# Performance work log

Measured on AMD Instinct MI355X. Metric: run time of the kernel, lower is better.

## Reference

```python
import jax, jax.numpy as jnp
import numpy as np

DIM = 768
N_HEADS = 12
HEAD_DIM = DIM // N_HEADS
B, S = 2, 4096


def setup_inputs() -> dict:
    key = jax.random.key(0)
    k_x, k_wqkv, k_bqkv, k_wout, k_bout = jax.random.split(key, 5)
    scale_in = 1.0 / np.sqrt(DIM)
    return {
        "x": jax.random.normal(k_x, (B, S, DIM), dtype=jnp.float32),
        "Wqkv": jax.random.normal(k_wqkv, (DIM, 3 * DIM), dtype=jnp.float32) * scale_in,
        "bqkv": jax.random.normal(k_bqkv, (3 * DIM,), dtype=jnp.float32) * 0.02,
        "Wout": jax.random.normal(k_wout, (DIM, DIM), dtype=jnp.float32) * scale_in,
        "bout": jax.random.normal(k_bout, (DIM,), dtype=jnp.float32) * 0.02,
    }


def reference(x, Wqkv, bqkv, Wout, bout):
    b, s, d = x.shape
    qkv = (x @ Wqkv + bqkv).reshape(b, s, 3, N_HEADS, HEAD_DIM)
    qkv = jnp.transpose(qkv, (2, 0, 3, 1, 4))  # [3, B, H, S, hd]
    q, k, v = qkv[0], qkv[1], qkv[2]
    scale = HEAD_DIM ** -0.5
    attn = jnp.einsum('bhqd,bhkd->bhqk', q, k) * scale  # [B, H, S, S]
    causal_mask = jnp.triu(jnp.ones((s, s), dtype=bool), k=1)
    attn = jnp.where(causal_mask[None, None], -jnp.inf, attn)
    attn = jax.nn.softmax(attn, axis=-1)
    out = jnp.einsum('bhqk,bhkd->bhqd', attn, v)  # [B, H, S, hd]
    out = jnp.transpose(out, (0, 2, 1, 3)).reshape(b, s, d)
    return out @ Wout + bout
```

## Files before the change

kernel.cpp:

```cpp
#include <hip/hip_runtime.h>
#include <hip/hip_bf16.h>
#include <math.h>

#define DIM 768
#define NH 12
#define HD 64
#define BATCH 2
#define SEQ 4096
#define MTOT (BATCH * SEQ)

#define QSCALE 0.1803368801111244f

typedef unsigned short u16;
typedef __bf16 bf16x8 __attribute__((ext_vector_type(8)));
typedef float  f32x4  __attribute__((ext_vector_type(4)));
typedef float  f32x16 __attribute__((ext_vector_type(16)));
typedef unsigned short u16x4 __attribute__((ext_vector_type(4)));
typedef unsigned short u16x8 __attribute__((ext_vector_type(8)));
typedef unsigned u32x4 __attribute__((ext_vector_type(4)));

__device__ inline u16 f2bf(float f) {
    unsigned u = __builtin_bit_cast(unsigned, f);
    u += 0x7fffu + ((u >> 16) & 1u);
    return (u16)(u >> 16);
}

#if defined(__has_builtin) && __has_builtin(__builtin_amdgcn_cvt_pk_bf16_f32)
#define HAVE_PK_BF16 1
__device__ inline unsigned pk2bf(float a, float b) {
    auto v = __builtin_amdgcn_cvt_pk_bf16_f32(a, b);
    return __builtin_bit_cast(unsigned, v);
}
#else
#define HAVE_PK_BF16 0
__device__ inline unsigned pk2bf(float a, float b) {
    return (unsigned)f2bf(a) | ((unsigned)f2bf(b) << 16);
}
#endif

__device__ inline f32x4 mfma16(bf16x8 a, bf16x8 b, f32x4 c) {
    return __builtin_amdgcn_mfma_f32_16x16x32_bf16(a, b, c, 0, 0, 0);
}
__device__ inline f32x16 mfma32(bf16x8 a, bf16x8 b, f32x16 c) {
    return __builtin_amdgcn_mfma_f32_32x32x16_bf16(a, b, c, 0, 0, 0);
}

__device__ inline void gl2lds16(const u16* g, u16* l) {
    __builtin_amdgcn_global_load_lds(
        (const __attribute__((address_space(1))) void*)g,
        (__attribute__((address_space(3))) void*)l,
        16, 0, 0);
}

__global__ __launch_bounds__(256)
void cvt_bf16(const float* __restrict__ src, u16* __restrict__ dst, int n8)
{
    int i = blockIdx.x * 256 + threadIdx.x;
    if (i >= n8) return;
    float4 a = ((const float4*)src)[i * 2];
    float4 b = ((const float4*)src)[i * 2 + 1];
    u16x8 o;
    o[0] = f2bf(a.x); o[1] = f2bf(a.y); o[2] = f2bf(a.z); o[3] = f2bf(a.w);
    o[4] = f2bf(b.x); o[5] = f2bf(b.y); o[6] = f2bf(b.z); o[7] = f2bf(b.w);
    ((u16x8*)dst)[i] = o;
}

__global__ __launch_bounds__(256)
void transpose_to_bf16(const float* __restrict__ src, u16* __restrict__ dst,
                       int R, int C)
{
    __shared__ float tile[32][33];
    const int c0 = blockIdx.x * 32, r0 = blockIdx.y * 32;
    const int tx = threadIdx.x & 31, ty = threadIdx.x >> 5;
#pragma unroll
    for (int i = 0; i < 4; ++i) {
        int row = ty * 4 + i;
        tile[row][tx] = src[(size_t)(r0 + row) * C + c0 + tx];
    }
    __syncthreads();
#pragma unroll
    for (int i = 0; i < 4; ++i) {
        int crow = ty * 4 + i;
        dst[(size_t)(c0 + crow) * R + r0 + tx] = f2bf(tile[tx][crow]);
    }
}

__device__ inline void gemm_lds_mainloop(const u16* __restrict__ Ag,
                                         const u16* __restrict__ Bg,
                                         int m0, int n0, int w, int lane,
                                         u16 (*As)[64 * 64], u16 (*Bs)[64 * 64],
                                         f32x4 acc[4][4])
{
    const int quad = lane >> 4, lc = lane & 15;
    const int wm = (w & 1) * 64, wn = (w >> 1) * 64;
    const int drow = lane >> 3;
    const int dp   = lane & 7;

#pragma unroll
    for (int mi = 0; mi < 4; ++mi)
#pragma unroll
        for (int nj = 0; nj < 4; ++nj)
            acc[mi][nj] = f32x4{0.f, 0.f, 0.f, 0.f};

#pragma unroll
    for (int i = 0; i < 2; ++i) {
        const int r  = w * 16 + i * 8 + drow;
        const int g  = dp ^ (r & 7);
        const int tr = 2 * r + (g >> 2);
        const int kc = g & 3;
        gl2lds16(Ag + (size_t)(m0 + tr) * 768 + kc * 8, &As[0][(w * 16 + i * 8) * 64]);
        gl2lds16(Bg + (size_t)(n0 + tr) * 768 + kc * 8, &Bs[0][(w * 16 + i * 8) * 64]);
    }
    __syncthreads();

    for (int ks = 0; ks < 24; ++ks) {
        const int cur = ks & 1;

        if (ks < 23) {
            const int k0n = (ks + 1) * 32;
#pragma unroll
            for (int i = 0; i < 2; ++i) {
                const int r  = w * 16 + i * 8 + drow;
                const int g  = dp ^ (r & 7);
                const int tr = 2 * r + (g >> 2);
                const int kc = g & 3;
                gl2lds16(Ag + (size_t)(m0 + tr) * 768 + k0n + kc * 8,
                         &As[1 - cur][(w * 16 + i * 8) * 64]);
                gl2lds16(Bg + (size_t)(n0 + tr) * 768 + k0n + kc * 8,
                         &Bs[1 - cur][(w * 16 + i * 8) * 64]);
            }
        }

        bf16x8 af[4], bfr[4];
#pragma unroll
        for (int mi = 0; mi < 4; ++mi) {
            const int m = wm + mi * 16 + lc;
            const int r = m >> 1;
            const int p = (((m & 1) * 4 + quad)) ^ (r & 7);
            af[mi] = *(const bf16x8*)&As[cur][r * 64 + p * 8];
        }
#pragma unroll
        for (int nj = 0; nj < 4; ++nj) {
            const int n = wn + nj * 16 + lc;
            const int r = n >> 1;
            const int p = (((n & 1) * 4 + quad)) ^ (r & 7);
            bfr[nj] = *(const bf16x8*)&Bs[cur][r * 64 + p * 8];
        }

#pragma unroll
        for (int mi = 0; mi < 4; ++mi)
#pragma unroll
            for (int nj = 0; nj < 4; ++nj)
                acc[mi][nj] = mfma16(af[mi], bfr[nj], acc[mi][nj]);

        __syncthreads();
    }
}

__global__ __launch_bounds__(256)
void gemm_qkv_mfma(const u16* __restrict__ A, const u16* __restrict__ Bt,
                   const float* __restrict__ bias,
                   u16* __restrict__ Qb, u16* __restrict__ Kb, u16* __restrict__ Vt)
{
    __shared__ u16 As[2][64 * 64];
    __shared__ u16 Bs[2][64 * 64];
    const int m0 = blockIdx.x * 128;
    const int n0 = blockIdx.y * 128;
    const int t = threadIdx.x;
    const int w = t >> 6, lane = t & 63;
    const int quad = lane >> 4, lc = lane & 15;
    const int wm = (w & 1) * 64, wn = (w >> 1) * 64;

    f32x4 acc[4][4];
    gemm_lds_mainloop(A, Bt, m0, n0, w, lane, As, Bs, acc);

    const int b  = m0 >> 12;
    const int s0 = (m0 & 4095) + wm;
    const int nbase = n0 + wn;
    const int three = nbase / 768;
    const int rem   = nbase - three * 768;
    const int h     = rem >> 6;
    const int bh    = b * NH + h;

    if (three < 2) {
        u16* dst = (three == 0) ? Qb : Kb;
        const float qs = (three == 0) ? QSCALE : 1.0f;
#pragma unroll
        for (int nj = 0; nj < 4; ++nj) {
            const float bi = bias[nbase + nj * 16 + lc];
            const int d = nj * 16 + lc;
#pragma unroll
            for (int mi = 0; mi < 4; ++mi) {
                const int s = s0 + mi * 16 + quad * 4;
#pragma unroll
                for (int r = 0; r < 4; ++r)
                    dst[((size_t)bh * SEQ + s + r) * HD + d] = f2bf((acc[mi][nj][r] + bi) * qs);
            }
        }
    } else {
#pragma unroll
        for (int nj = 0; nj < 4; ++nj) {
            const float bi = bias[nbase + nj * 16 + lc];
            const int d = nj * 16 + lc;
            const size_t rowb = ((size_t)bh * HD + d) * SEQ;
#pragma unroll
            for (int mi = 0; mi < 4; ++mi) {
                const int s = s0 + mi * 16 + quad * 4;
                u16x4 wv;
#pragma unroll
                for (int r = 0; r < 4; ++r) wv[r] = f2bf(acc[mi][nj][r] + bi);
                *(u16x4*)&Vt[rowb + s] = wv;
            }
        }
    }
}

__global__ __launch_bounds__(256)
void gemm_out_mfma(const u16* __restrict__ A, const u16* __restrict__ Bt,
                   const float* __restrict__ bias, float* __restrict__ C)
{
    __shared__ u16 As[2][64 * 64];
    __shared__ u16 Bs[2][64 * 64];
    const int m0 = blockIdx.x * 128;
    const int n0 = blockIdx.y * 128;
    const int t = threadIdx.x;
    const int w = t >> 6, lane = t & 63;
    const int quad = lane >> 4, lc = lane & 15;
    const int wm = (w & 1) * 64, wn = (w >> 1) * 64;

    f32x4 acc[4][4];
    gemm_lds_mainloop(A, Bt, m0, n0, w, lane, As, Bs, acc);

#pragma unroll
    for (int nj = 0; nj < 4; ++nj) {
        const int col = n0 + wn + nj * 16 + lc;
        const float bi = bias[col];
#pragma unroll
        for (int mi = 0; mi < 4; ++mi) {
            const int row = m0 + wm + mi * 16 + quad * 4;
#pragma unroll
            for (int r = 0; r < 4; ++r)
                C[(size_t)(row + r) * 768 + col] = acc[mi][nj][r] + bi;
        }
    }
}

__global__ __launch_bounds__(256, 3)
void flash_attn(const u16* __restrict__ Qg, const u16* __restrict__ Kg,
                const u16* __restrict__ Vtg, u16* __restrict__ Og)
{
    const int bh   = blockIdx.x;
    const int pair = blockIdx.y;
    const int b    = bh / NH, h = bh % NH;
    const int t    = threadIdx.x;
    const int w    = t >> 6;
    const int wq   = w >> 1;
    const int wk   = w & 1;
    const int lane = t & 63;
    const int lc32 = lane & 31;
    const int hi   = lane >> 5;
    const int drow = lane >> 3;
    const int dp   = lane & 7;

    __shared__ u16 Ks[3][64 * 64];
    __shared__ u16 Vs[3][64 * 64];

    const u16* Qp = Qg  + (size_t)bh * SEQ * HD;
    const u16* Kp = Kg  + (size_t)bh * SEQ * HD;
    const u16* Vp = Vtg + (size_t)bh * HD * SEQ;
    float* Vscr = (float*)&Vs[0][0];
    float* Lx   = (float*)&Ks[0][0];

#pragma unroll 1
    for (int half = 0; half < 2; ++half) {
        const int qt    = half ? pair : (63 - pair);
        const int qrow0 = qt * 64 + wq * 32;

#pragma unroll
        for (int i = 0; i < 2; ++i) {
            const int r0  = w * 16 + i * 8;
            const int row = r0 + drow;
            const int gc  = dp ^ (row & 7);
            gl2lds16(Kp + (size_t)row * HD + gc * 8, &Ks[0][r0 * 64]);
            gl2lds16(Vp + (size_t)row * SEQ + gc * 8, &Vs[0][r0 * 64]);
        }
        if (qt >= 1) {
#pragma unroll
            for (int i = 0; i < 2; ++i) {
                const int r0  = w * 16 + i * 8;
                const int row = r0 + drow;
                const int gc  = dp ^ (row & 7);
                gl2lds16(Kp + (size_t)(64 + row) * HD + gc * 8, &Ks[1][r0 * 64]);
                gl2lds16(Vp + (size_t)row * SEQ + 64 + gc * 8, &Vs[1][r0 * 64]);
            }
        }

        bf16x8 qa[4];
#pragma unroll
        for (int ds = 0; ds < 4; ++ds)
            qa[ds] = *(const bf16x8*)
                &Qp[(size_t)(qrow0 + lc32) * HD + ds * 16 + hi * 8];

        f32x16 o2[2];
        o2[0] = f32x16{};
        o2[1] = f32x16{};
        float l_r = 0.f;

        if (qt >= 1) { asm volatile("s_waitcnt vmcnt(8)" ::: "memory"); }
        else         { asm volatile("s_waitcnt vmcnt(4)" ::: "memory"); }
        __builtin_amdgcn_s_barrier();

        int cur = 0;
        for (int tk = 0; tk <= qt; ++tk) {
            const int kb = tk * 64;

            if (tk + 2 <= qt) {
                const int kb2 = kb + 128;
                const int nb  = (cur >= 1) ? (cur - 1) : 2;
#pragma unroll
                for (int i = 0; i < 2; ++i) {
                    const int r0  = w * 16 + i * 8;
                    const int row = r0 + drow;
                    const int gc  = dp ^ (row & 7);
                    gl2lds16(Kp + (size_t)(kb2 + row) * HD + gc * 8,
                             &Ks[nb][r0 * 64]);
                    gl2lds16(Vp + (size_t)row * SEQ + kb2 + gc * 8,
                             &Vs[nb][r0 * 64]);
                }
            }

            f32x16 sacc = {};
            {
                const int row = wk * 32 + lc32;
                const int sw  = row & 7;
#pragma unroll
                for (int ds = 0; ds < 4; ++ds) {
                    bf16x8 kf = *(const bf16x8*)
                        &Ks[cur][row * 64 + (((ds * 2 + hi) ^ sw) * 8)];
                    sacc = mfma32(kf, qa[ds], sacc);
                }
            }

            if (tk == qt) {
                const int q = qrow0 + lc32;
#pragma unroll
                for (int r = 0; r < 16; ++r) {
                    const int key = kb + wk * 32 + (r & 3) + 8 * (r >> 2) + 4 * hi;
                    if (key > q) sacc[r] = -1e30f;
                }
            }

            float pv[16];
#pragma unroll
            for (int r = 0; r < 16; ++r)
                pv[r] = __builtin_amdgcn_exp2f(sacc[r]);

            l_r += (((pv[0] + pv[1]) + (pv[2] + pv[3]))
                  + ((pv[4] + pv[5]) + (pv[6] + pv[7])))
                 + (((pv[8] + pv[9]) + (pv[10] + pv[11]))
                  + ((pv[12] + pv[13]) + (pv[14] + pv[15])));

            bf16x8 pa[2];
#pragma unroll
            for (int s = 0; s < 2; ++s) {
                unsigned w0 = pk2bf(pv[8 * s + 0], pv[8 * s + 1]);
                unsigned w1 = pk2bf(pv[8 * s + 2], pv[8 * s + 3]);
                unsigned w2 = pk2bf(pv[8 * s + 4], pv[8 * s + 5]);
                unsigned w3 = pk2bf(pv[8 * s + 6], pv[8 * s + 7]);
                asm("v_permlane32_swap_b32 %0, %1" : "+v"(w0), "+v"(w2));
                asm("v_permlane32_swap_b32 %0, %1" : "+v"(w1), "+v"(w3));
                u32x4 tw;
                tw[0] = w0; tw[1] = w1; tw[2] = w2; tw[3] = w3;
                pa[s] = __builtin_bit_cast(bf16x8, tw);
            }

#pragma unroll
            for (int dt = 0; dt < 2; ++dt) {
                const int row = dt * 32 + lc32;
                const int sw  = row & 7;
#pragma unroll
                for (int s = 0; s < 2; ++s) {
                    bf16x8 vf = *(const bf16x8*)
                        &Vs[cur][row * 64 + (((wk * 4 + s * 2 + hi) ^ sw) * 8)];
                    o2[dt] = mfma32(pa[s], vf, o2[dt]);
                }
            }

            if (tk + 2 <= qt) { asm volatile("s_waitcnt vmcnt(4)" ::: "memory"); }
            else              { asm volatile("s_waitcnt vmcnt(0)" ::: "memory"); }
            __builtin_amdgcn_s_barrier();

            cur = (cur == 2) ? 0 : cur + 1;
        }

        const float lt = l_r + __shfl_xor(l_r, 32);

        if (wk == 1) {
#pragma unroll
            for (int dt = 0; dt < 2; ++dt)
#pragma unroll
                for (int r = 0; r < 16; ++r) {
                    const int ql = (r & 3) + 8 * (r >> 2) + 4 * hi;
                    Vscr[wq * 2048 + ql * 64 + dt * 32 + lc32] = o2[dt][r];
                }
            if (lane < 32) Lx[wq * 32 + lc32] = lt;
        }
        __syncthreads();
        if (wk == 0) {
            const float linv_q = 1.0f / (lt + Lx[wq * 32 + lc32]);
#pragma unroll
            for (int r = 0; r < 16; ++r) {
                const int ql   = (r & 3) + 8 * (r >> 2) + 4 * hi;
                const float li = __shfl(linv_q, ql);
                const int q = qrow0 + ql;
                const size_t base = ((size_t)(b * SEQ + q)) * DIM + h * HD + lc32;
#pragma unroll
                for (int dt = 0; dt < 2; ++dt) {
                    const float ov = o2[dt][r]
                        + Vscr[wq * 2048 + ql * 64 + dt * 32 + lc32];
                    Og[base + dt * 32] = f2bf(ov * li);
                }
            }
        }
        __syncthreads();
    }
}

extern "C" void kernel_launch(void* const* d_in, const int* in_sizes, int n_in,
                              void* d_out, int out_size, void* d_ws, size_t ws_size,
                              hipStream_t stream)
{
    const float* x    = (const float*)d_in[0];
    const float* Wqkv = (const float*)d_in[1];
    const float* bqkv = (const float*)d_in[2];
    const float* Wout = (const float*)d_in[3];
    const float* bout = (const float*)d_in[4];
    float* out = (float*)d_out;

    const size_t NX  = (size_t)MTOT * DIM;
    const size_t NWQ = (size_t)DIM * 3 * DIM;
    const size_t NWO = (size_t)DIM * DIM;
    u16* p   = (u16*)d_ws;
    u16* Xb  = p;              p += NX;
    u16* Wqt = p;              p += NWQ;
    u16* Wot = p;              p += NWO;
    u16* Qb  = p;              p += NX;
    u16* Kb  = p;              p += NX;
    u16* Vt  = p;              p += NX;
    u16* Ao  = p;

    cvt_bf16<<<(int)(NX / 8 + 255) / 256, 256, 0, stream>>>(x, Xb, (int)(NX / 8));
    transpose_to_bf16<<<dim3(2304 / 32, 768 / 32), 256, 0, stream>>>(Wqkv, Wqt, 768, 2304);
    transpose_to_bf16<<<dim3(768 / 32, 768 / 32), 256, 0, stream>>>(Wout, Wot, 768, 768);

    gemm_qkv_mfma<<<dim3(MTOT / 128, 2304 / 128), 256, 0, stream>>>(Xb, Wqt, bqkv, Qb, Kb, Vt);
    flash_attn<<<dim3(24, 32), 256, 0, stream>>>(Qb, Kb, Vt, Ao);
    gemm_out_mfma<<<dim3(MTOT / 128, 768 / 128), 256, 0, stream>>>(Ao, Wot, bout, out);
}
```

Baseline: 242.7 us.

## Software-pipeline QK^T of next tile with softmax/PV of current tile

Restructures the causal attention inner loop so that the QK^T MFMA for key tile tk+1 is issued before the exp/softmax and PV MFMAs of tile tk, with two score accumulators alternating between iterations. The intent is to overlap the transcendental and VALU work with matrix-core work. Three changes come together: the Q fragment loads are hoisted ahead of the second K/V prefetch, the barrier and waitcnt placement is reorganised around a rotating triple buffer, and s_setprio is raised around MFMA blocks. The cost is more live registers for a second 16-float score accumulator, and a full vmcnt(0) wait each step that may expose load latency.

```diff
diff --git a/kernel.cpp b/kernel.cpp
--- a/kernel.cpp
+++ b/kernel.cpp
@@ -271,6 +271,9 @@
     float* Vscr = (float*)&Vs[0][0];
     float* Lx   = (float*)&Ks[0][0];
 
+    const int krow = wk * 32 + lc32;
+    const int ksw  = krow & 7;
+
 #pragma unroll 1
     for (int half = 0; half < 2; ++half) {
         const int qt    = half ? pair : (63 - pair);
@@ -284,6 +287,13 @@
             gl2lds16(Kp + (size_t)row * HD + gc * 8, &Ks[0][r0 * 64]);
             gl2lds16(Vp + (size_t)row * SEQ + gc * 8, &Vs[0][r0 * 64]);
         }
+
+        bf16x8 qa[4];
+#pragma unroll
+        for (int ds = 0; ds < 4; ++ds)
+            qa[ds] = *(const bf16x8*)
+                &Qp[(size_t)(qrow0 + lc32) * HD + ds * 16 + hi * 8];
+
         if (qt >= 1) {
 #pragma unroll
             for (int i = 0; i < 2; ++i) {
@@ -295,65 +305,73 @@
             }
         }
 
-        bf16x8 qa[4];
-#pragma unroll
-        for (int ds = 0; ds < 4; ++ds)
-            qa[ds] = *(const bf16x8*)
-                &Qp[(size_t)(qrow0 + lc32) * HD + ds * 16 + hi * 8];
-
         f32x16 o2[2];
         o2[0] = f32x16{};
         o2[1] = f32x16{};
         float l_r = 0.f;
 
-        if (qt >= 1) { asm volatile("s_waitcnt vmcnt(8)" ::: "memory"); }
-        else         { asm volatile("s_waitcnt vmcnt(4)" ::: "memory"); }
+        if (qt >= 1) { asm volatile("s_waitcnt vmcnt(4)" ::: "memory"); }
+        else         { asm volatile("s_waitcnt vmcnt(0)" ::: "memory"); }
         __builtin_amdgcn_s_barrier();
 
-        int cur = 0;
-        for (int tk = 0; tk <= qt; ++tk) {
+        auto maskf = [&](f32x16& s, int kb) {
+            const int q = qrow0 + lc32;
+#pragma unroll
+            for (int r = 0; r < 16; ++r) {
+                const int key = kb + wk * 32 + (r & 3) + 8 * (r >> 2) + 4 * hi;
+                if (key > q) s[r] = -1e30f;
+            }
+        };
+
+        f32x16 s0 = {}, s1 = {};
+        {
+            __builtin_amdgcn_s_setprio(1);
+#pragma unroll
+            for (int ds = 0; ds < 4; ++ds) {
+                bf16x8 kf = *(const bf16x8*)
+                    &Ks[0][krow * 64 + (((ds * 2 + hi) ^ ksw) * 8)];
+                s0 = mfma32(kf, qa[ds], s0);
+            }
+            __builtin_amdgcn_s_setprio(0);
+        }
+        if (qt == 0) maskf(s0, 0);
+
+        int cb = 0, nb = 1, db = 2;
+
+        auto step = [&](f32x16& scur, f32x16& snxt, int tk) {
             const int kb = tk * 64;
-
-            if (tk + 2 <= qt) {
-                const int kb2 = kb + 128;
-                const int nb  = (cur >= 1) ? (cur - 1) : 2;
-#pragma unroll
-                for (int i = 0; i < 2; ++i) {
-                    const int r0  = w * 16 + i * 8;
-                    const int row = r0 + drow;
-                    const int gc  = dp ^ (row & 7);
-                    gl2lds16(Kp + (size_t)(kb2 + row) * HD + gc * 8,
-                             &Ks[nb][r0 * 64]);
-                    gl2lds16(Vp + (size_t)row * SEQ + kb2 + gc * 8,
-                             &Vs[nb][r0 * 64]);
+            if (tk + 1 <= qt) {
+                asm volatile("s_waitcnt vmcnt(0)" ::: "memory");
+                __builtin_amdgcn_s_barrier();
+                if (tk + 2 <= qt) {
+                    const int kb2 = kb + 128;
+#pragma unroll
+                    for (int i = 0; i < 2; ++i) {
+                        const int r0  = w * 16 + i * 8;
+                        const int row = r0 + drow;
+                        const int gc  = dp ^ (row & 7);
+                        gl2lds16(Kp + (size_t)(kb2 + row) * HD + gc * 8,
+                                 &Ks[db][r0 * 64]);
+                        gl2lds16(Vp + (size_t)row * SEQ + kb2 + gc * 8,
+                                 &Vs[db][r0 * 64]);
+                    }
                 }
-            }
-
-            f32x16 sacc = {};
-            {
-                const int row = wk * 32 + lc32;
-                const int sw  = row & 7;
+                snxt = f32x16{};
+                __builtin_amdgcn_s_setprio(1);
 #pragma unroll
                 for (int ds = 0; ds < 4; ++ds) {
                     bf16x8 kf = *(const bf16x8*)
-                        &Ks[cur][row * 64 + (((ds * 2 + hi) ^ sw) * 8)];
-                    sacc = mfma32(kf, qa[ds], sacc);
+                        &Ks[nb][krow * 64 + (((ds * 2 + hi) ^ ksw) * 8)];
+                    snxt = mfma32(kf, qa[ds], snxt);
                 }
-            }
-
-            if (tk == qt) {
-                const int q = qrow0 + lc32;
-#pragma unroll
-                for (int r = 0; r < 16; ++r) {
-                    const int key = kb + wk * 32 + (r & 3) + 8 * (r >> 2) + 4 * hi;
-                    if (key > q) sacc[r] = -1e30f;
-                }
+                __builtin_amdgcn_s_setprio(0);
+                if (tk + 1 == qt) maskf(snxt, kb + 64);
             }
 
             float pv[16];
 #pragma unroll
             for (int r = 0; r < 16; ++r)
-                pv[r] = __builtin_amdgcn_exp2f(sacc[r]);
+                pv[r] = __builtin_amdgcn_exp2f(scur[r]);
 
             l_r += (((pv[0] + pv[1]) + (pv[2] + pv[3]))
                   + ((pv[4] + pv[5]) + (pv[6] + pv[7])))
@@ -374,6 +392,7 @@
                 pa[s] = __builtin_bit_cast(bf16x8, tw);
             }
 
+            __builtin_amdgcn_s_setprio(1);
 #pragma unroll
             for (int dt = 0; dt < 2; ++dt) {
                 const int row = dt * 32 + lc32;
@@ -381,17 +400,21 @@
 #pragma unroll
                 for (int s = 0; s < 2; ++s) {
                     bf16x8 vf = *(const bf16x8*)
-                        &Vs[cur][row * 64 + (((wk * 4 + s * 2 + hi) ^ sw) * 8)];
+                        &Vs[cb][row * 64 + (((wk * 4 + s * 2 + hi) ^ sw) * 8)];
                     o2[dt] = mfma32(pa[s], vf, o2[dt]);
                 }
             }
-
-            if (tk + 2 <= qt) { asm volatile("s_waitcnt vmcnt(4)" ::: "memory"); }
-            else              { asm volatile("s_waitcnt vmcnt(0)" ::: "memory"); }
-            __builtin_amdgcn_s_barrier();
-
-            cur = (cur == 2) ? 0 : cur + 1;
-        }
+            __builtin_amdgcn_s_setprio(0);
+        };
+
+#pragma unroll 1
+        for (int tk = 0; tk <= qt; ++tk) {
+            if ((tk & 1) == 0) step(s0, s1, tk);
+            else               step(s1, s0, tk);
+            const int tmp = cb; cb = nb; nb = db; db = tmp;
+        }
+
+        __syncthreads();
 
         const float lt = l_r + __shfl_xor(l_r, 32);
 
```

Measured after the change: 304.3 us. 1.25x slower.
